# Optimization experiments

Measured on AMD Instinct MI355X. Metric: run time of the kernel, lower is better.

The kernel has to match this reference:

```python
import jax, jax.numpy as jnp
import numpy as np

HEAD = 16  # from init_kwargs
NEG_FILL = -1e20


def setup_inputs() -> dict:
    key = jax.random.key(0)
    ks = jax.random.split(key, 6)
    N, S, E = 4, 2048, 1024
    D = E // HEAD  # 64
    value = jax.random.normal(ks[0], (N, S, E), dtype=jnp.float32)
    key_t = jax.random.normal(ks[1], (N, S, E), dtype=jnp.float32)
    query = jax.random.normal(ks[2], (N, S, E), dtype=jnp.float32)
    # multiplicative causal mask broadcastable to (N, H, S, S)
    mask = jnp.tril(jnp.ones((S, S), dtype=jnp.float32))[None, None, :, :]
    # per-head-dim projection weights (Dense(head_dim) applied after reshape,
    # so weights are (D, D), shared across heads) -- faithful to source
    sc = 1.0 / np.sqrt(D)
    Wq = jax.random.normal(ks[3], (D, D), dtype=jnp.float32) * sc
    Wk = jax.random.normal(ks[4], (D, D), dtype=jnp.float32) * sc
    Wv = jax.random.normal(ks[5], (D, D), dtype=jnp.float32) * sc
    return {"value": value, "key": key_t, "query": query, "mask": mask,
            "Wq": Wq, "Wk": Wk, "Wv": Wv}


def reference(value, key, query, mask, Wq, Wk, Wv):
    N, Lq, E = query.shape
    H = HEAD
    D = E // H
    # reshape to heads, then project last dim (D -> D)
    q = jnp.einsum('nqhd,de->nqhe', query.reshape(N, Lq, H, D), Wq)
    k = jnp.einsum('nkhd,de->nkhe', key.reshape(N, key.shape[1], H, D), Wk)
    v = jnp.einsum('nvhd,de->nvhe', value.reshape(N, value.shape[1], H, D), Wv)
    # unscaled QK^T (source has no 1/sqrt(d))
    energy = jnp.einsum('nqhd,nkhd->nhqk', q, k)  # (N,H,Lq,Lk)
    energy = energy * mask
    energy = jnp.where(energy == 0, NEG_FILL, energy)
    attention = jax.nn.softmax(energy, axis=-1)
    out = jnp.einsum('nhql,nlhd->nqhd', attention, v).reshape(N, Lq, H * D)
    return out  # fc_layer defined in __init__ but never used in call()
```

## Files before the change

kernel.cpp:

```cpp
#include <hip/hip_runtime.h>
#include <hip/hip_bf16.h>
#include <math.h>


#define NB  4
#define SEQ 2048
#define HD  16
#define DH  64
#define NH  (NB*HD)

typedef _Float16 half8  __attribute__((ext_vector_type(8)));
typedef _Float16 half2  __attribute__((ext_vector_type(2)));
typedef __fp16   fp16x2 __attribute__((ext_vector_type(2)));
typedef float    f32x4  __attribute__((ext_vector_type(4)));
typedef float    f32x16 __attribute__((ext_vector_type(16)));

__device__ inline half2 pkrtz(float a, float b) {
  union { fp16x2 f; half2 h; } u;
  u.f = __builtin_amdgcn_cvt_pkrtz(a, b);
  return u.h;
}

__device__ inline void gload16(const void* g, void* l) {
  __builtin_amdgcn_global_load_lds(
      (const __attribute__((address_space(1))) void*)g,
      (__attribute__((address_space(3))) void*)l, 16, 0, 0);
}

__global__ __launch_bounds__(256) void proj_kernel(
    const float* __restrict__ q_in, const float* __restrict__ k_in,
    const float* __restrict__ v_in,
    const float* __restrict__ Wq, const float* __restrict__ Wk,
    const float* __restrict__ Wv,
    _Float16* __restrict__ Qp, _Float16* __restrict__ Kp,
    _Float16* __restrict__ Vt)
{
  __shared__ float Wl[64*64];
  const int t = threadIdx.x;
  const int which = blockIdx.z;
  const float* in = which == 0 ? q_in : (which == 1 ? k_in : v_in);
  const float* W  = which == 0 ? Wq   : (which == 1 ? Wk   : Wv);

  const int nh = blockIdx.y;
  const int n = nh >> 4, h = nh & 15;
  const int s0 = blockIdx.x * 256;

  #pragma unroll
  for (int i = 0; i < 16; ++i) Wl[i*256 + t] = W[i*256 + t];
  __syncthreads();

  const int w = t >> 6, lane = t & 63, lr = lane & 15, lg = lane >> 4;

  if (which < 2) {
    const float oscale = (which == 0) ? 1.44269504088896f : 1.0f;
    half8 bfr[4][2];
    #pragma unroll
    for (int g = 0; g < 4; ++g)
      #pragma unroll
      for (int kc = 0; kc < 2; ++kc)
        #pragma unroll
        for (int i = 0; i < 8; ++i)
          bfr[g][kc][i] = (_Float16)Wl[(kc*32 + lg*8 + i)*64 + 16*g + lr];

    _Float16* outp = (which == 0 ? Qp : Kp) + (size_t)nh*SEQ*DH;
    #pragma unroll
    for (int pass = 0; pass < 4; ++pass) {
      int row0 = s0 + (pass*4 + w)*16;
      const float* ip = in + ((size_t)(n*SEQ + row0 + lr))*(HD*DH) + h*DH;
      float4 a0 = *(const float4*)(ip + lg*8);
      float4 a1 = *(const float4*)(ip + lg*8 + 4);
      float4 a2 = *(const float4*)(ip + 32 + lg*8);
      float4 a3 = *(const float4*)(ip + 32 + lg*8 + 4);
      half8 af0, af1;
      af0[0]=(_Float16)a0.x; af0[1]=(_Float16)a0.y; af0[2]=(_Float16)a0.z; af0[3]=(_Float16)a0.w;
      af0[4]=(_Float16)a1.x; af0[5]=(_Float16)a1.y; af0[6]=(_Float16)a1.z; af0[7]=(_Float16)a1.w;
      af1[0]=(_Float16)a2.x; af1[1]=(_Float16)a2.y; af1[2]=(_Float16)a2.z; af1[3]=(_Float16)a2.w;
      af1[4]=(_Float16)a3.x; af1[5]=(_Float16)a3.y; af1[6]=(_Float16)a3.z; af1[7]=(_Float16)a3.w;
      f32x4 c[4] = {{0,0,0,0},{0,0,0,0},{0,0,0,0},{0,0,0,0}};
      #pragma unroll
      for (int g = 0; g < 4; ++g) {
        c[g] = __builtin_amdgcn_mfma_f32_16x16x32_f16(af0, bfr[g][0], c[g], 0, 0, 0);
        c[g] = __builtin_amdgcn_mfma_f32_16x16x32_f16(af1, bfr[g][1], c[g], 0, 0, 0);
      }
      #pragma unroll
      for (int g = 0; g < 4; ++g)
        #pragma unroll
        for (int j = 0; j < 4; ++j)
          outp[(size_t)(row0 + 4*lg + j)*DH + 16*g + lr] =
              (_Float16)(c[g][j] * oscale);
    }
  } else {
    half8 afr[2];
    #pragma unroll
    for (int kc = 0; kc < 2; ++kc)
      #pragma unroll
      for (int i = 0; i < 8; ++i)
        afr[kc][i] = (_Float16)Wl[(kc*32 + lg*8 + i)*64 + w*16 + lr];

    _Float16* outp = Vt + (size_t)nh*DH*SEQ;
    #pragma unroll
    for (int pass = 0; pass < 4; ++pass) {
      int sc0 = s0 + pass*64;
      f32x4 c[4] = {{0,0,0,0},{0,0,0,0},{0,0,0,0},{0,0,0,0}};
      #pragma unroll
      for (int g = 0; g < 4; ++g) {
        const float* ip = in + ((size_t)(n*SEQ + sc0 + 16*g + lr))*(HD*DH) + h*DH;
        float4 b0 = *(const float4*)(ip + lg*8);
        float4 b1 = *(const float4*)(ip + lg*8 + 4);
        float4 b2 = *(const float4*)(ip + 32 + lg*8);
        float4 b3 = *(const float4*)(ip + 32 + lg*8 + 4);
        half8 bf0, bf1;
        bf0[0]=(_Float16)b0.x; bf0[1]=(_Float16)b0.y; bf0[2]=(_Float16)b0.z; bf0[3]=(_Float16)b0.w;
        bf0[4]=(_Float16)b1.x; bf0[5]=(_Float16)b1.y; bf0[6]=(_Float16)b1.z; bf0[7]=(_Float16)b1.w;
        bf1[0]=(_Float16)b2.x; bf1[1]=(_Float16)b2.y; bf1[2]=(_Float16)b2.z; bf1[3]=(_Float16)b2.w;
        bf1[4]=(_Float16)b3.x; bf1[5]=(_Float16)b3.y; bf1[6]=(_Float16)b3.z; bf1[7]=(_Float16)b3.w;
        c[g] = __builtin_amdgcn_mfma_f32_16x16x32_f16(afr[0], bf0, c[g], 0, 0, 0);
        c[g] = __builtin_amdgcn_mfma_f32_16x16x32_f16(afr[1], bf1, c[g], 0, 0, 0);
      }
      #pragma unroll
      for (int g = 0; g < 4; ++g)
        #pragma unroll
        for (int j = 0; j < 4; ++j) {
          int kcol = 16*g + lr;
          int pcol = (kcol & ~12) | ((kcol & 8) >> 1) | ((kcol & 4) << 1);
          outp[(size_t)(w*16 + 4*lg + j)*SEQ + sc0 + pcol] = (_Float16)c[g][j];
        }
    }
  }
}

#define STAGEG(buf, ktn)                                          \
  do {                                                            \
    _Float16* kd = &lds[buf][g][0][0];                            \
    _Float16* vd = &lds[buf][g][1][0];                            \
    gload16(kg + (size_t)(ktn)*DH,         kd + gtid*8);          \
    gload16(kg + (size_t)(ktn)*DH + 32*DH, kd + (256+gtid)*8);    \
    gload16(vg + (ktn),                    vd + gtid*8);          \
    gload16(vg + (ktn) + 32*SEQ,           vd + (256+gtid)*8);    \
  } while (0)

#define MERGE_OUT(Q0W)                                                      \
  do {                                                                      \
    unsigned* ov = (unsigned*)&lds[cur][0][0][0];                           \
    float invl = lsum > 0.f ? 1.f/lsum : 0.f;                               \
    if (g == 1) {                                                           \
      unsigned* pp = ov + (wi*64 + lane)*18;                                \
      _Pragma("unroll")                                                     \
      for (int jj = 0; jj < 8; ++jj) {                                      \
        union { half2 h; unsigned u; } u0, u1;                              \
        u0.h = pkrtz(o0[2*jj]*invl, o0[2*jj+1]*invl);                       \
        u1.h = pkrtz(o1[2*jj]*invl, o1[2*jj+1]*invl);                       \
        pp[jj] = u0.u; pp[8+jj] = u1.u;                                     \
      }                                                                     \
      union { float f; unsigned u; } um, ul;                                \
      um.f = m; ul.f = lsum;                                                \
      pp[16] = um.u; pp[17] = ul.u;                                         \
    }                                                                       \
    __syncthreads();                                                        \
    if (g == 0) {                                                           \
      const unsigned* pp = ov + (wi*64 + lane)*18;                          \
      union { float f; unsigned u; } um, ul;                                \
      um.u = pp[16]; ul.u = pp[17];                                         \
      float m1 = um.f, l1 = ul.f;                                           \
      float mf = fmaxf(m, m1);                                              \
      float wa = lsum * exp2f(m - mf);                                      \
      float wb = (l1 > 0.f ? l1 : 0.f) * exp2f(m1 - mf);                    \
      float invd = 1.f / (wa + wb);                                         \
      float ca = wa * invl * invd;                                          \
      float cb = wb * invd;                                                 \
      float* orow = out + ((size_t)n*SEQ + (Q0W) + lq)*(HD*DH) + h*DH;      \
      _Pragma("unroll")                                                     \
      for (int jj = 0; jj < 8; ++jj) {                                      \
        union { unsigned u; half2 h; } v0, v1;                              \
        v0.u = pp[jj]; v1.u = pp[8+jj];                                     \
        int j0 = 2*jj, j1 = 2*jj + 1;                                       \
        int dl0 = 4*lg1 + 8*(j0>>2) + (j0&3);                               \
        int dl1 = 4*lg1 + 8*(j1>>2) + (j1&3);                               \
        orow[dl0]      = ca*o0[j0] + cb*(float)v0.h[0];                     \
        orow[dl1]      = ca*o0[j1] + cb*(float)v0.h[1];                     \
        orow[32 + dl0] = ca*o1[j0] + cb*(float)v1.h[0];                     \
        orow[32 + dl1] = ca*o1[j1] + cb*(float)v1.h[1];                     \
      }                                                                     \
    }                                                                       \
    __syncthreads();                                                        \
  } while (0)

__global__ __launch_bounds__(512, 4) void attn_kernel(
    const _Float16* __restrict__ Qp,
    const _Float16* __restrict__ Kp,
    const _Float16* __restrict__ Vt,
    float* __restrict__ out)
{
  __shared__ __attribute__((aligned(16))) _Float16 lds[2][2][2][4096];

  const int bid  = blockIdx.x;
  const int head = bid & 63;
  const int p    = bid >> 6;
  const int n = head >> 4, h = head & 15;
  const int tid = threadIdx.x;
  const int w8 = tid >> 6;
  const int g  = w8 >> 2;
  const int wi = w8 & 3;
  const int lane = tid & 63;
  const int lq = lane & 31, lg1 = lane >> 5;
  const int gtid = tid & 255;

  const int TmaxA = 2*p + 1;
  const int q0A = p*128 + wi*32;
  const int q0B = (15 - p)*128 + wi*32;
  const int TwA = (q0A >> 6);
  const int TwB = (q0B >> 6);

  const _Float16* Kbase = Kp + (size_t)head*SEQ*DH;
  const _Float16* Vbase = Vt + (size_t)head*DH*SEQ;

  const _Float16* QrowA = Qp + ((size_t)head*SEQ + q0A + lq)*DH + 8*lg1;
  const _Float16* QrowB = Qp + ((size_t)head*SEQ + q0B + lq)*DH + 8*lg1;
  half8 qf[4];
  #pragma unroll
  for (int c = 0; c < 4; ++c) qf[c] = *(const half8*)(QrowA + 16*c);

  int roff[2][4];
  #pragma unroll
  for (int rt = 0; rt < 2; ++rt)
    #pragma unroll
    for (int c = 0; c < 4; ++c)
      roff[rt][c] = (32*rt + lq)*128 + (((2*c + lg1) ^ (lq & 7)) << 4);

  const int srow = gtid >> 3;
  const int scs  = (gtid & 7) ^ (srow & 7);
  const _Float16* kg = Kbase + (size_t)srow*DH + scs*8;
  const _Float16* vg = Vbase + (size_t)srow*SEQ + scs*8;

  float m = -INFINITY, lsum = 0.f;
  f32x16 o0 = {0,0,0,0,0,0,0,0,0,0,0,0,0,0,0,0};
  f32x16 o1 = {0,0,0,0,0,0,0,0,0,0,0,0,0,0,0,0};

  STAGEG(0, g*64);

  int cur = 0;
  for (int i = 0; i <= 16; ++i) {
    if (i < 16) {
      const int Gn  = 2*(i + 1) + g;
      const int ktn = (Gn <= TmaxA ? Gn : Gn - TmaxA - 1) * 64;
      STAGEG(cur^1, ktn);
      asm volatile("s_waitcnt vmcnt(4)" ::: "memory");
    } else {
      asm volatile("s_waitcnt vmcnt(0)" ::: "memory");
    }
    __builtin_amdgcn_sched_barrier(0);
    __builtin_amdgcn_s_barrier();
    __builtin_amdgcn_sched_barrier(0);

    const int G    = 2*i + g;
    const bool phA = (G <= TmaxA);
    const int  tt  = phA ? G : G - TmaxA - 1;
    const int  Tw  = phA ? TwA : TwB;

    if (tt <= Tw) {
      const char* Kb = (const char*)&lds[cur][g][0][0];
      const char* Vb = (const char*)&lds[cur][g][1][0];
      const int kt = tt*64;
      const int q  = (phA ? q0A : q0B) + lq;

      f32x16 s0 = {0,0,0,0,0,0,0,0,0,0,0,0,0,0,0,0};
      f32x16 s1 = {0,0,0,0,0,0,0,0,0,0,0,0,0,0,0,0};
      __builtin_amdgcn_s_setprio(1);
      #pragma unroll
      for (int c = 0; c < 4; ++c) {
        half8 ka = *(const half8*)(Kb + roff[0][c]);
        half8 kb = *(const half8*)(Kb + roff[1][c]);
        s0 = __builtin_amdgcn_mfma_f32_32x32x16_f16(ka, qf[c], s0, 0, 0, 0);
        s1 = __builtin_amdgcn_mfma_f32_32x32x16_f16(kb, qf[c], s1, 0, 0, 0);
      }
      __builtin_amdgcn_s_setprio(0);
      if (tt == Tw) {
        #pragma unroll
        for (int j = 0; j < 16; ++j) {
          int kl = 4*lg1 + 8*(j>>2) + (j&3);
          if (kt + kl      > q) s0[j] = -1e30f;
          if (kt + 32 + kl > q) s1[j] = -1e30f;
        }
      }
      float t0[8];
      #pragma unroll
      for (int j = 0; j < 8; ++j)
        t0[j] = fmaxf(fmaxf(s0[j], s0[j+8]), fmaxf(s1[j], s1[j+8]));
      float pm = fmaxf(fmaxf(fmaxf(t0[0],t0[1]), fmaxf(t0[2],t0[3])),
                       fmaxf(fmaxf(t0[4],t0[5]), fmaxf(t0[6],t0[7])));
      pm = fmaxf(pm, __shfl_xor(pm, 32));
      if (!__all(pm <= m + 8.f)) {
        float mn = fmaxf(m, pm);
        float sc = exp2f(m - mn);
        m = mn;
        lsum *= sc;
        #pragma unroll
        for (int j = 0; j < 16; ++j) { o0[j] *= sc; o1[j] *= sc; }
      }
      #pragma unroll
      for (int j = 0; j < 16; ++j) {
        s0[j] = exp2f(s0[j] - m);
        s1[j] = exp2f(s1[j] - m);
      }
      float u0[8];
      #pragma unroll
      for (int j = 0; j < 8; ++j)
        u0[j] = (s0[j] + s0[j+8]) + (s1[j] + s1[j+8]);
      float ps = ((u0[0]+u0[1]) + (u0[2]+u0[3])) + ((u0[4]+u0[5]) + (u0[6]+u0[7]));
      ps += __shfl_xor(ps, 32);
      lsum += ps;

      half2 pkA[8], pkB[8];
      #pragma unroll
      for (int jj = 0; jj < 8; ++jj) {
        pkA[jj] = pkrtz(s0[2*jj], s0[2*jj+1]);
        pkB[jj] = pkrtz(s1[2*jj], s1[2*jj+1]);
      }
      __builtin_amdgcn_s_setprio(1);
      #pragma unroll
      for (int c = 0; c < 4; ++c) {
        union { half8 hh; half2 pp[4]; } pb;
        pb.pp[0] = (c < 2) ? pkA[(c&1)*4 + 0] : pkB[(c&1)*4 + 0];
        pb.pp[1] = (c < 2) ? pkA[(c&1)*4 + 1] : pkB[(c&1)*4 + 1];
        pb.pp[2] = (c < 2) ? pkA[(c&1)*4 + 2] : pkB[(c&1)*4 + 2];
        pb.pp[3] = (c < 2) ? pkA[(c&1)*4 + 3] : pkB[(c&1)*4 + 3];
        half8 va = *(const half8*)(Vb + roff[0][c]);
        half8 vb = *(const half8*)(Vb + roff[1][c]);
        o0 = __builtin_amdgcn_mfma_f32_32x32x16_f16(va, pb.hh, o0, 0, 0, 0);
        o1 = __builtin_amdgcn_mfma_f32_32x32x16_f16(vb, pb.hh, o1, 0, 0, 0);
      }
      __builtin_amdgcn_s_setprio(0);
    }

    __builtin_amdgcn_sched_barrier(0);
    __builtin_amdgcn_s_barrier();

    if (i == p) {
      MERGE_OUT(q0A);
      m = -INFINITY; lsum = 0.f;
      #pragma unroll
      for (int j = 0; j < 16; ++j) { o0[j] = 0.f; o1[j] = 0.f; }
      #pragma unroll
      for (int c = 0; c < 4; ++c) qf[c] = *(const half8*)(QrowB + 16*c);
    }
    if (i < 16) cur ^= 1;
  }

  MERGE_OUT(q0B);
}

extern "C" void kernel_launch(void* const* d_in, const int* in_sizes, int n_in,
                              void* d_out, int out_size, void* d_ws, size_t ws_size,
                              hipStream_t stream) {
  (void)in_sizes; (void)n_in; (void)out_size; (void)ws_size;
  const float* value = (const float*)d_in[0];
  const float* key   = (const float*)d_in[1];
  const float* query = (const float*)d_in[2];
  const float* Wq = (const float*)d_in[4];
  const float* Wk = (const float*)d_in[5];
  const float* Wv = (const float*)d_in[6];

  _Float16* Qp = (_Float16*)d_ws;
  _Float16* Kp = Qp + (size_t)NH*SEQ*DH;
  _Float16* Vt = Kp + (size_t)NH*SEQ*DH;
  float* out = (float*)d_out;

  proj_kernel<<<dim3(8, 64, 3), 256, 0, stream>>>(query, key, value,
                                                  Wq, Wk, Wv, Qp, Kp, Vt);
  attn_kernel<<<dim3(512), 512, 0, stream>>>(Qp, Kp, Vt, out);
}
```

Baseline: 106.5 us.

## Halve key tile to 32 and shrink LDS to double occupancy

Processes 32 keys per tile instead of 64, halving the LDS staging buffers, and raises launch bounds to 8 blocks per CU. Tile indexing, V layout offsets and causal skipping are rewritten for the finer granularity, and the output merge is split into two passes so it fits the smaller LDS. The intent is higher occupancy and less wasted work on the diagonal. In exchange it doubles the iteration count and the per-iteration barriers, gives less MFMA work per tile, and adds merge synchronisations.

After: 256.9 us. 2.41x slower.

```diff
diff --git a/kernel.cpp b/kernel.cpp
--- a/kernel.cpp
+++ b/kernel.cpp
@@ -133,51 +133,68 @@
   do {                                                            \
     _Float16* kd = &lds[buf][g][0][0];                            \
     _Float16* vd = &lds[buf][g][1][0];                            \
-    gload16(kg + (size_t)(ktn)*DH,         kd + gtid*8);          \
-    gload16(kg + (size_t)(ktn)*DH + 32*DH, kd + (256+gtid)*8);    \
-    gload16(vg + (ktn),                    vd + gtid*8);          \
-    gload16(vg + (ktn) + 32*SEQ,           vd + (256+gtid)*8);    \
+    gload16(kg + (size_t)(ktn)*DH, kd + gtid*8);                  \
+    gload16(vg + (ktn),            vd + gtid*8);                  \
   } while (0)
 
 #define MERGE_OUT(Q0W)                                                      \
   do {                                                                      \
     unsigned* ov = (unsigned*)&lds[cur][0][0][0];                           \
+    unsigned* pp = ov + (wi*64 + lane)*10;                                  \
     float invl = lsum > 0.f ? 1.f/lsum : 0.f;                               \
+    float ca = 0.f, cb = 0.f;                                               \
+    float* orow = out + ((size_t)n*SEQ + (Q0W) + lq)*(HD*DH) + h*DH;        \
     if (g == 1) {                                                           \
-      unsigned* pp = ov + (wi*64 + lane)*18;                                \
       _Pragma("unroll")                                                     \
       for (int jj = 0; jj < 8; ++jj) {                                      \
-        union { half2 h; unsigned u; } u0, u1;                              \
+        union { half2 h; unsigned u; } u0;                                  \
         u0.h = pkrtz(o0[2*jj]*invl, o0[2*jj+1]*invl);                       \
-        u1.h = pkrtz(o1[2*jj]*invl, o1[2*jj+1]*invl);                       \
-        pp[jj] = u0.u; pp[8+jj] = u1.u;                                     \
+        pp[jj] = u0.u;                                                      \
       }                                                                     \
       union { float f; unsigned u; } um, ul;                                \
       um.f = m; ul.f = lsum;                                                \
-      pp[16] = um.u; pp[17] = ul.u;                                         \
+      pp[8] = um.u; pp[9] = ul.u;                                           \
     }                                                                       \
     __syncthreads();                                                        \
     if (g == 0) {                                                           \
-      const unsigned* pp = ov + (wi*64 + lane)*18;                          \
       union { float f; unsigned u; } um, ul;                                \
-      um.u = pp[16]; ul.u = pp[17];                                         \
+      um.u = pp[8]; ul.u = pp[9];                                           \
       float m1 = um.f, l1 = ul.f;                                           \
       float mf = fmaxf(m, m1);                                              \
       float wa = lsum * exp2f(m - mf);                                      \
       float wb = (l1 > 0.f ? l1 : 0.f) * exp2f(m1 - mf);                    \
       float invd = 1.f / (wa + wb);                                         \
-      float ca = wa * invl * invd;                                          \
-      float cb = wb * invd;                                                 \
-      float* orow = out + ((size_t)n*SEQ + (Q0W) + lq)*(HD*DH) + h*DH;      \
+      ca = wa * invl * invd;                                                \
+      cb = wb * invd;                                                       \
       _Pragma("unroll")                                                     \
       for (int jj = 0; jj < 8; ++jj) {                                      \
-        union { unsigned u; half2 h; } v0, v1;                              \
-        v0.u = pp[jj]; v1.u = pp[8+jj];                                     \
+        union { unsigned u; half2 h; } v0;                                  \
+        v0.u = pp[jj];                                                      \
         int j0 = 2*jj, j1 = 2*jj + 1;                                       \
         int dl0 = 4*lg1 + 8*(j0>>2) + (j0&3);                               \
         int dl1 = 4*lg1 + 8*(j1>>2) + (j1&3);                               \
-        orow[dl0]      = ca*o0[j0] + cb*(float)v0.h[0];                     \
-        orow[dl1]      = ca*o0[j1] + cb*(float)v0.h[1];                     \
+        orow[dl0] = ca*o0[j0] + cb*(float)v0.h[0];                          \
+        orow[dl1] = ca*o0[j1] + cb*(float)v0.h[1];                          \
+      }                                                                     \
+    }                                                                       \
+    __syncthreads();                                                        \
+    if (g == 1) {                                                           \
+      _Pragma("unroll")                                                     \
+      for (int jj = 0; jj < 8; ++jj) {                                      \
+        union { half2 h; unsigned u; } u1;                                  \
+        u1.h = pkrtz(o1[2*jj]*invl, o1[2*jj+1]*invl);                       \
+        pp[jj] = u1.u;                                                      \
+      }                                                                     \
+    }                                                                       \
+    __syncthreads();                                                        \
+    if (g == 0) {                                                           \
+      _Pragma("unroll")                                                     \
+      for (int jj = 0; jj < 8; ++jj) {                                      \
+        union { unsigned u; half2 h; } v1;                                  \
+        v1.u = pp[jj];                                                      \
+        int j0 = 2*jj, j1 = 2*jj + 1;                                       \
+        int dl0 = 4*lg1 + 8*(j0>>2) + (j0&3);                               \
+        int dl1 = 4*lg1 + 8*(j1>>2) + (j1&3);                               \
         orow[32 + dl0] = ca*o1[j0] + cb*(float)v1.h[0];                     \
         orow[32 + dl1] = ca*o1[j1] + cb*(float)v1.h[1];                     \
       }                                                                     \
@@ -185,13 +202,13 @@
     __syncthreads();                                                        \
   } while (0)
 
-__global__ __launch_bounds__(512, 4) void attn_kernel(
+__global__ __launch_bounds__(512, 8) void attn_kernel(
     const _Float16* __restrict__ Qp,
     const _Float16* __restrict__ Kp,
     const _Float16* __restrict__ Vt,
     float* __restrict__ out)
 {
-  __shared__ __attribute__((aligned(16))) _Float16 lds[2][2][2][4096];
+  __shared__ __attribute__((aligned(16))) _Float16 lds[2][2][2][2048];
 
   const int bid  = blockIdx.x;
   const int head = bid & 63;
@@ -205,11 +222,12 @@
   const int lq = lane & 31, lg1 = lane >> 5;
   const int gtid = tid & 255;
 
-  const int TmaxA = 2*p + 1;
   const int q0A = p*128 + wi*32;
   const int q0B = (15 - p)*128 + wi*32;
-  const int TwA = (q0A >> 6);
-  const int TwB = (q0B >> 6);
+  const int TwA = 4*p + wi;
+  const int TwB = 4*(15 - p) + wi;
+  const int iA  = 2*p + 1;
+  const int nTA = 4*p + 4;
 
   const _Float16* Kbase = Kp + (size_t)head*SEQ*DH;
   const _Float16* Vbase = Vt + (size_t)head*DH*SEQ;
@@ -220,31 +238,36 @@
   #pragma unroll
   for (int c = 0; c < 4; ++c) qf[c] = *(const half8*)(QrowA + 16*c);
 
-  int roff[2][4];
+  int koff[4];
   #pragma unroll
-  for (int rt = 0; rt < 2; ++rt)
-    #pragma unroll
-    for (int c = 0; c < 4; ++c)
-      roff[rt][c] = (32*rt + lq)*128 + (((2*c + lg1) ^ (lq & 7)) << 4);
+  for (int c = 0; c < 4; ++c)
+    koff[c] = lq*128 + (((2*c + lg1) ^ (lq & 7)) << 4);
+  int voff[2][2];
+  #pragma unroll
+  for (int ho = 0; ho < 2; ++ho)
+    #pragma unroll
+    for (int kc = 0; kc < 2; ++kc)
+      voff[ho][kc] = lq*128 + (((ho*4 + kc*2 + lg1) ^ (lq & 7)) << 4);
 
   const int srow = gtid >> 3;
   const int scs  = (gtid & 7) ^ (srow & 7);
   const _Float16* kg = Kbase + (size_t)srow*DH + scs*8;
-  const _Float16* vg = Vbase + (size_t)srow*SEQ + scs*8;
+  const int dv = srow + ((scs >= 4) ? 32 : 0);
+  const _Float16* vg = Vbase + (size_t)dv*SEQ + (scs & 3)*8;
 
   float m = -INFINITY, lsum = 0.f;
   f32x16 o0 = {0,0,0,0,0,0,0,0,0,0,0,0,0,0,0,0};
   f32x16 o1 = {0,0,0,0,0,0,0,0,0,0,0,0,0,0,0,0};
 
-  STAGEG(0, g*64);
+  STAGEG(0, g*32);
 
   int cur = 0;
-  for (int i = 0; i <= 16; ++i) {
-    if (i < 16) {
+  for (int i = 0; i <= 33; ++i) {
+    if (i < 33) {
       const int Gn  = 2*(i + 1) + g;
-      const int ktn = (Gn <= TmaxA ? Gn : Gn - TmaxA - 1) * 64;
+      const int ktn = ((i + 1 <= iA) ? Gn : Gn - nTA) * 32;
       STAGEG(cur^1, ktn);
-      asm volatile("s_waitcnt vmcnt(4)" ::: "memory");
+      asm volatile("s_waitcnt vmcnt(2)" ::: "memory");
     } else {
       asm volatile("s_waitcnt vmcnt(0)" ::: "memory");
     }
@@ -252,40 +275,34 @@
     __builtin_amdgcn_s_barrier();
     __builtin_amdgcn_sched_barrier(0);
 
-    const int G    = 2*i + g;
-    const bool phA = (G <= TmaxA);
-    const int  tt  = phA ? G : G - TmaxA - 1;
+    const bool phA = (i <= iA);
+    const int  tt  = phA ? (2*i + g) : (2*i + g - nTA);
     const int  Tw  = phA ? TwA : TwB;
 
     if (tt <= Tw) {
       const char* Kb = (const char*)&lds[cur][g][0][0];
       const char* Vb = (const char*)&lds[cur][g][1][0];
-      const int kt = tt*64;
+      const int kt = tt*32;
       const int q  = (phA ? q0A : q0B) + lq;
 
       f32x16 s0 = {0,0,0,0,0,0,0,0,0,0,0,0,0,0,0,0};
-      f32x16 s1 = {0,0,0,0,0,0,0,0,0,0,0,0,0,0,0,0};
       __builtin_amdgcn_s_setprio(1);
       #pragma unroll
       for (int c = 0; c < 4; ++c) {
-        half8 ka = *(const half8*)(Kb + roff[0][c]);
-        half8 kb = *(const half8*)(Kb + roff[1][c]);
+        half8 ka = *(const half8*)(Kb + koff[c]);
         s0 = __builtin_amdgcn_mfma_f32_32x32x16_f16(ka, qf[c], s0, 0, 0, 0);
-        s1 = __builtin_amdgcn_mfma_f32_32x32x16_f16(kb, qf[c], s1, 0, 0, 0);
       }
       __builtin_amdgcn_s_setprio(0);
       if (tt == Tw) {
         #pragma unroll
         for (int j = 0; j < 16; ++j) {
           int kl = 4*lg1 + 8*(j>>2) + (j&3);
-          if (kt + kl      > q) s0[j] = -1e30f;
-          if (kt + 32 + kl > q) s1[j] = -1e30f;
+          if (kt + kl > q) s0[j] = -1e30f;
         }
       }
       float t0[8];
       #pragma unroll
-      for (int j = 0; j < 8; ++j)
-        t0[j] = fmaxf(fmaxf(s0[j], s0[j+8]), fmaxf(s1[j], s1[j+8]));
+      for (int j = 0; j < 8; ++j) t0[j] = fmaxf(s0[j], s0[j+8]);
       float pm = fmaxf(fmaxf(fmaxf(t0[0],t0[1]), fmaxf(t0[2],t0[3])),
                        fmaxf(fmaxf(t0[4],t0[5]), fmaxf(t0[6],t0[7])));
       pm = fmaxf(pm, __shfl_xor(pm, 32));
@@ -298,34 +315,29 @@
         for (int j = 0; j < 16; ++j) { o0[j] *= sc; o1[j] *= sc; }
       }
       #pragma unroll
-      for (int j = 0; j < 16; ++j) {
-        s0[j] = exp2f(s0[j] - m);
-        s1[j] = exp2f(s1[j] - m);
-      }
+      for (int j = 0; j < 16; ++j) s0[j] = exp2f(s0[j] - m);
       float u0[8];
       #pragma unroll
-      for (int j = 0; j < 8; ++j)
-        u0[j] = (s0[j] + s0[j+8]) + (s1[j] + s1[j+8]);
+      for (int j = 0; j < 8; ++j) u0[j] = s0[j] + s0[j+8];
       float ps = ((u0[0]+u0[1]) + (u0[2]+u0[3])) + ((u0[4]+u0[5]) + (u0[6]+u0[7]));
       ps += __shfl_xor(ps, 32);
       lsum += ps;
 
-      half2 pkA[8], pkB[8];
-      #pragma unroll
-      for (int jj = 0; jj < 8; ++jj) {
-        pkA[jj] = pkrtz(s0[2*jj], s0[2*jj+1]);
-        pkB[jj] = pkrtz(s1[2*jj], s1[2*jj+1]);
-      }
+      half2 pk[8];
+      #pragma unroll
+      for (int jj = 0; jj < 8; ++jj)
+        pk[jj] = pkrtz(s0[2*jj], s0[2*jj+1]);
+
       __builtin_amdgcn_s_setprio(1);
       #pragma unroll
-      for (int c = 0; c < 4; ++c) {
+      for (int kc = 0; kc < 2; ++kc) {
         union { half8 hh; half2 pp[4]; } pb;
-        pb.pp[0] = (c < 2) ? pkA[(c&1)*4 + 0] : pkB[(c&1)*4 + 0];
-        pb.pp[1] = (c < 2) ? pkA[(c&1)*4 + 1] : pkB[(c&1)*4 + 1];
-        pb.pp[2] = (c < 2) ? pkA[(c&1)*4 + 2] : pkB[(c&1)*4 + 2];
-        pb.pp[3] = (c < 2) ? pkA[(c&1)*4 + 3] : pkB[(c&1)*4 + 3];
-        half8 va = *(const half8*)(Vb + roff[0][c]);
-        half8 vb = *(const half8*)(Vb + roff[1][c]);
+        pb.pp[0] = pk[kc*4 + 0];
+        pb.pp[1] = pk[kc*4 + 1];
+        pb.pp[2] = pk[kc*4 + 2];
+        pb.pp[3] = pk[kc*4 + 3];
+        half8 va = *(const half8*)(Vb + voff[0][kc]);
+        half8 vb = *(const half8*)(Vb + voff[1][kc]);
         o0 = __builtin_amdgcn_mfma_f32_32x32x16_f16(va, pb.hh, o0, 0, 0, 0);
         o1 = __builtin_amdgcn_mfma_f32_32x32x16_f16(vb, pb.hh, o1, 0, 0, 0);
       }
@@ -335,7 +347,7 @@
     __builtin_amdgcn_sched_barrier(0);
     __builtin_amdgcn_s_barrier();
 
-    if (i == p) {
+    if (i == iA) {
       MERGE_OUT(q0A);
       m = -INFINITY; lsum = 0.f;
       #pragma unroll
@@ -343,7 +355,7 @@
       #pragma unroll
       for (int c = 0; c < 4; ++c) qf[c] = *(const half8*)(QrowB + 16*c);
     }
-    if (i < 16) cur ^= 1;
+    if (i < 33) cur ^= 1;
   }
 
   MERGE_OUT(q0B);
```
